# Optimization experiments

Measured on AMD Instinct MI355X. Metric: run time of the kernel, lower is better.

The kernel has to match this reference:

```python
import jax, jax.numpy as jnp
import numpy as np

NUM_HEADS = 32
NUM_GROUP_HEADS = 8
DIM_MODEL = 2048
DIM_K = 64
DIM_V = 64


def setup_inputs() -> dict:
    key = jax.random.key(0)
    ks = jax.random.split(key, 11)
    B, S = 1, 2048
    scale = 0.02
    inp = {
        "queries": jax.random.normal(ks[0], (B, S, DIM_MODEL), jnp.float32),
        "keys": jax.random.normal(ks[1], (B, S, DIM_MODEL), jnp.float32),
        "values": jax.random.normal(ks[2], (B, S, DIM_MODEL), jnp.float32),
        "Wq": jax.random.normal(ks[3], (DIM_MODEL, DIM_K * NUM_HEADS), jnp.float32) * scale,
        "bq": jnp.zeros((DIM_K * NUM_HEADS,), jnp.float32),
        "Wk": jax.random.normal(ks[4], (DIM_MODEL, DIM_K * NUM_GROUP_HEADS), jnp.float32) * scale,
        "bk": jnp.zeros((DIM_K * NUM_GROUP_HEADS,), jnp.float32),
        "Wv": jax.random.normal(ks[5], (DIM_MODEL, DIM_V * NUM_GROUP_HEADS), jnp.float32) * scale,
        "bv": jnp.zeros((DIM_V * NUM_GROUP_HEADS,), jnp.float32),
        "Wo": jax.random.normal(ks[6], (DIM_V * NUM_HEADS, DIM_MODEL), jnp.float32) * scale,
        "bo": jnp.zeros((DIM_MODEL,), jnp.float32),
    }
    return inp


def reference(queries, keys, values, Wq, bq, Wk, bk, Wv, bv, Wo, bo):
    B, Sq, _ = queries.shape
    _, Sk, _ = keys.shape
    H, G = NUM_HEADS, NUM_GROUP_HEADS
    repeats = H // G

    # projections -> [B, heads, S, d]
    q = (queries @ Wq + bq).reshape(B, Sq, H, DIM_K).transpose(0, 2, 1, 3)
    k = (keys @ Wk + bk).reshape(B, Sk, G, DIM_K).transpose(0, 2, 1, 3)
    v = (values @ Wv + bv).reshape(B, Sk, G, DIM_V).transpose(0, 2, 1, 3)

    # GQA: repeat each group head `repeats` times (repeat_interleave on head dim)
    k = jnp.repeat(k, repeats, axis=1)  # [B, H, Sk, dk]
    v = jnp.repeat(v, repeats, axis=1)  # [B, H, Sk, dv]

    scores = jnp.einsum("bhqd,bhkd->bhqk", q, k) / (DIM_K ** 0.5)
    causal = jnp.triu(jnp.ones((Sq, Sk), dtype=bool), k=1)
    scores = jnp.where(causal, -jnp.inf, scores)
    attn = jax.nn.softmax(scores, axis=-1)
    out = jnp.einsum("bhqk,bhkd->bhqd", attn, v)  # [B, H, Sq, dv]
    out = out.transpose(0, 2, 1, 3).reshape(B, Sq, H * DIM_V)
    return out @ Wo + bo
```

## Files before the change

### kernel.cpp

```cpp
#include <hip/hip_runtime.h>
#include <hip/hip_bf16.h>

#define S_LEN  2048
#define DMODEL 2048
#define NH     32
#define NG     8
#define DK     64
#define DV     64

typedef short bf16x8 __attribute__((ext_vector_type(8)));
typedef float f32x4  __attribute__((ext_vector_type(4)));

__device__ __forceinline__ ushort f32_to_bf16(float f) {
    uint u = __float_as_uint(f);
    return (ushort)((u + 0x7fffu + ((u >> 16) & 1u)) >> 16);
}
__device__ __forceinline__ float bf16_to_f32(ushort h) {
    return __uint_as_float(((uint)h) << 16);
}
__device__ __forceinline__ uint pack_bf16x2(float a, float b) {
    return (uint)f32_to_bf16(a) | ((uint)f32_to_bf16(b) << 16);
}

__global__ void cast3_f32_to_bf16(const float* __restrict__ q,
                                  const float* __restrict__ k,
                                  const float* __restrict__ v,
                                  ushort* __restrict__ xq,
                                  ushort* __restrict__ xk,
                                  ushort* __restrict__ xv, int n8) {
    const float* in  = blockIdx.z == 0 ? q  : (blockIdx.z == 1 ? k  : v);
    ushort*      out = blockIdx.z == 0 ? xq : (blockIdx.z == 1 ? xk : xv);
    int i = blockIdx.x * blockDim.x + threadIdx.x;
    const int stride = gridDim.x * blockDim.x;
    for (; i < n8; i += stride) {
        const float4 a = ((const float4*)in)[2 * i];
        const float4 b = ((const float4*)in)[2 * i + 1];
        uint4 o;
        o.x = (uint)f32_to_bf16(a.x) | ((uint)f32_to_bf16(a.y) << 16);
        o.y = (uint)f32_to_bf16(a.z) | ((uint)f32_to_bf16(a.w) << 16);
        o.z = (uint)f32_to_bf16(b.x) | ((uint)f32_to_bf16(b.y) << 16);
        o.w = (uint)f32_to_bf16(b.z) | ((uint)f32_to_bf16(b.w) << 16);
        ((uint4*)out)[i] = o;
    }
}

__global__ void transpose_cast4(const float* __restrict__ Wq,
                                const float* __restrict__ Wk,
                                const float* __restrict__ Wv,
                                const float* __restrict__ Wo,
                                ushort* __restrict__ Wqt, ushort* __restrict__ Wkt,
                                ushort* __restrict__ Wvt, ushort* __restrict__ Wot) {
    __shared__ float t[32][33];
    int bx = blockIdx.x;
    const float* W; ushort* Wt; int N;
    if (bx < 64)      { W = Wq; Wt = Wqt; N = 2048; }
    else if (bx < 80) { W = Wk; Wt = Wkt; N = 512;  bx -= 64; }
    else if (bx < 96) { W = Wv; Wt = Wvt; N = 512;  bx -= 80; }
    else              { W = Wo; Wt = Wot; N = 2048; bx -= 96; }
    const int n0 = bx * 32, k0 = blockIdx.y * 32;
    const int tx = threadIdx.x, ty = threadIdx.y;
#pragma unroll
    for (int i = 0; i < 4; ++i)
        t[ty + 8 * i][tx] = W[(size_t)(k0 + ty + 8 * i) * N + n0 + tx];
    __syncthreads();
#pragma unroll
    for (int i = 0; i < 4; ++i)
        Wt[(size_t)(n0 + ty + 8 * i) * 2048 + k0 + tx] = f32_to_bf16(t[tx][ty + 8 * i]);
}

template <int MODE>
__device__ __forceinline__ void gemm_body_128x64(
        const ushort* __restrict__ A, const ushort* __restrict__ Bt,
        const float* __restrict__ bias, void* __restrict__ Cv,
        ushort* As, ushort* Bs, ushort* Ts, int N, int K, float scale,
        int bx, int by) {
    const int tid  = threadIdx.x;
    const int lane = tid & 63, wave = tid >> 6;
    const int l15 = lane & 15, quad = lane >> 4;
    const int row0 = by * 128, col0 = bx * 64;

    f32x4 acc[2][4];
#pragma unroll
    for (int i = 0; i < 2; ++i)
#pragma unroll
        for (int j = 0; j < 4; ++j) { f32x4 z = {0.f,0.f,0.f,0.f}; acc[i][j] = z; }

    const int ar = tid >> 1, ak = (tid & 1) * 32;
    const int br = tid >> 2, bk = (tid & 3) * 16;
    const ushort* aptr = A  + (size_t)(row0 + ar) * K + ak;
    const ushort* bptr = Bt + (size_t)(col0 + br) * K + bk;

    bf16x8 xa0 = *(const bf16x8*)(aptr);
    bf16x8 xa1 = *(const bf16x8*)(aptr + 8);
    bf16x8 xa2 = *(const bf16x8*)(aptr + 16);
    bf16x8 xa3 = *(const bf16x8*)(aptr + 24);
    bf16x8 xb0 = *(const bf16x8*)(bptr);
    bf16x8 xb1 = *(const bf16x8*)(bptr + 8);
    bf16x8 ya0 = *(const bf16x8*)(aptr + 64);
    bf16x8 ya1 = *(const bf16x8*)(aptr + 72);
    bf16x8 ya2 = *(const bf16x8*)(aptr + 80);
    bf16x8 ya3 = *(const bf16x8*)(aptr + 88);
    bf16x8 yb0 = *(const bf16x8*)(bptr + 64);
    bf16x8 yb1 = *(const bf16x8*)(bptr + 72);

    for (int k0 = 0; k0 < K; k0 += 128) {
        __syncthreads();
        *(bf16x8*)&As[ar * 72 + ak]      = xa0;
        *(bf16x8*)&As[ar * 72 + ak + 8]  = xa1;
        *(bf16x8*)&As[ar * 72 + ak + 16] = xa2;
        *(bf16x8*)&As[ar * 72 + ak + 24] = xa3;
        *(bf16x8*)&Bs[br * 72 + bk]      = xb0;
        *(bf16x8*)&Bs[br * 72 + bk + 8]  = xb1;
        __syncthreads();
        if (k0 + 128 < K) {
            xa0 = *(const bf16x8*)(aptr + k0 + 128);
            xa1 = *(const bf16x8*)(aptr + k0 + 136);
            xa2 = *(const bf16x8*)(aptr + k0 + 144);
            xa3 = *(const bf16x8*)(aptr + k0 + 152);
            xb0 = *(const bf16x8*)(bptr + k0 + 128);
            xb1 = *(const bf16x8*)(bptr + k0 + 136);
        }
#pragma unroll
        for (int kk = 0; kk < 2; ++kk) {
            bf16x8 af[2], bf[4];
#pragma unroll
            for (int mi = 0; mi < 2; ++mi)
                af[mi] = *(const bf16x8*)&As[(wave * 32 + mi * 16 + l15) * 72 + kk * 32 + quad * 8];
#pragma unroll
            for (int ni = 0; ni < 4; ++ni)
                bf[ni] = *(const bf16x8*)&Bs[(ni * 16 + l15) * 72 + kk * 32 + quad * 8];
#pragma unroll
            for (int mi = 0; mi < 2; ++mi)
#pragma unroll
                for (int ni = 0; ni < 4; ++ni)
                    acc[mi][ni] = __builtin_amdgcn_mfma_f32_16x16x32_bf16(
                        af[mi], bf[ni], acc[mi][ni], 0, 0, 0);
        }

        __syncthreads();
        *(bf16x8*)&As[ar * 72 + ak]      = ya0;
        *(bf16x8*)&As[ar * 72 + ak + 8]  = ya1;
        *(bf16x8*)&As[ar * 72 + ak + 16] = ya2;
        *(bf16x8*)&As[ar * 72 + ak + 24] = ya3;
        *(bf16x8*)&Bs[br * 72 + bk]      = yb0;
        *(bf16x8*)&Bs[br * 72 + bk + 8]  = yb1;
        __syncthreads();
        if (k0 + 192 < K) {
            ya0 = *(const bf16x8*)(aptr + k0 + 192);
            ya1 = *(const bf16x8*)(aptr + k0 + 200);
            ya2 = *(const bf16x8*)(aptr + k0 + 208);
            ya3 = *(const bf16x8*)(aptr + k0 + 216);
            yb0 = *(const bf16x8*)(bptr + k0 + 192);
            yb1 = *(const bf16x8*)(bptr + k0 + 200);
        }
#pragma unroll
        for (int kk = 0; kk < 2; ++kk) {
            bf16x8 af[2], bf[4];
#pragma unroll
            for (int mi = 0; mi < 2; ++mi)
                af[mi] = *(const bf16x8*)&As[(wave * 32 + mi * 16 + l15) * 72 + kk * 32 + quad * 8];
#pragma unroll
            for (int ni = 0; ni < 4; ++ni)
                bf[ni] = *(const bf16x8*)&Bs[(ni * 16 + l15) * 72 + kk * 32 + quad * 8];
#pragma unroll
            for (int mi = 0; mi < 2; ++mi)
#pragma unroll
                for (int ni = 0; ni < 4; ++ni)
                    acc[mi][ni] = __builtin_amdgcn_mfma_f32_16x16x32_bf16(
                        af[mi], bf[ni], acc[mi][ni], 0, 0, 0);
        }
    }

    if (MODE == 2) {
        __syncthreads();
#pragma unroll
        for (int mi = 0; mi < 2; ++mi)
#pragma unroll
            for (int ni = 0; ni < 4; ++ni) {
                const float bv = bias[col0 + ni * 16 + l15];
                const int lrow = wave * 32 + mi * 16 + quad * 4;
                uint2 uu;
                uu.x = pack_bf16x2((acc[mi][ni][0] + bv) * scale,
                                   (acc[mi][ni][1] + bv) * scale);
                uu.y = pack_bf16x2((acc[mi][ni][2] + bv) * scale,
                                   (acc[mi][ni][3] + bv) * scale);
                *(uint2*)&Ts[(ni * 16 + l15) * 136 + lrow] = uu;
            }
        __syncthreads();
        const int v = tid >> 2, s0 = (tid & 3) * 32;
#pragma unroll
        for (int i = 0; i < 4; ++i) {
            const uint4 d = *(const uint4*)&Ts[v * 136 + s0 + 8 * i];
            *(uint4*)&((ushort*)Cv)[(size_t)(col0 + v) * S_LEN + row0 + s0 + 8 * i] = d;
        }
        return;
    }

#pragma unroll
    for (int mi = 0; mi < 2; ++mi)
#pragma unroll
        for (int ni = 0; ni < 4; ++ni) {
            const int col = col0 + ni * 16 + l15;
            const float bv = bias[col];
#pragma unroll
            for (int reg = 0; reg < 4; ++reg) {
                const int row = row0 + wave * 32 + mi * 16 + quad * 4 + reg;
                const float val = (acc[mi][ni][reg] + bv) * scale;
                if (MODE == 1)
                    ((float*)Cv)[(size_t)row * N + col] = val;
                else
                    ((ushort*)Cv)[(size_t)row * N + col] = f32_to_bf16(val);
            }
        }
}

__device__ __forceinline__ void xcd_decode_32x16(int d, int& bx, int& by) {
    const int xcd = d & 7, i = d >> 3;
    bx = (xcd & 3) * 8 + (i & 7);
    by = (xcd >> 2) * 8 + (i >> 3);
}

__global__ __launch_bounds__(256) void gemm_q(
        const ushort* __restrict__ A, const ushort* __restrict__ Bt,
        const float* __restrict__ bias, ushort* __restrict__ Cv, int K,
        float scale) {
    __shared__ ushort smem[128 * 72 + 64 * 72];
    int bx, by; xcd_decode_32x16(blockIdx.x, bx, by);
    gemm_body_128x64<0>(A, Bt, bias, Cv, smem, smem + 128 * 72, nullptr,
                        2048, K, scale, bx, by);
}

__global__ __launch_bounds__(256) void gemm_o(
        const ushort* __restrict__ A, const ushort* __restrict__ Bt,
        const float* __restrict__ bias, float* __restrict__ Cv, int K) {
    __shared__ ushort smem[128 * 72 + 64 * 72];
    int bx, by; xcd_decode_32x16(blockIdx.x, bx, by);
    gemm_body_128x64<1>(A, Bt, bias, Cv, smem, smem + 128 * 72, nullptr,
                        2048, K, 1.0f, bx, by);
}

__global__ __launch_bounds__(256) void gemm_kv(
        const ushort* __restrict__ Xk, const ushort* __restrict__ Xv,
        const ushort* __restrict__ Wkt, const ushort* __restrict__ Wvt,
        const float* __restrict__ bk, const float* __restrict__ bv,
        ushort* __restrict__ Kb, ushort* __restrict__ Vtp, int K) {
    __shared__ ushort smem[128 * 72 + 64 * 72];
    ushort* As = smem;
    ushort* Bs = smem + 128 * 72;
    if (blockIdx.z == 0)
        gemm_body_128x64<0>(Xk, Wkt, bk, Kb, As, Bs, nullptr, 512, K, 1.0f,
                            blockIdx.x, blockIdx.y);
    else
        gemm_body_128x64<2>(Xv, Wvt, bv, Vtp, As, Bs, smem, 512, K, 1.0f,
                            blockIdx.x, blockIdx.y);
}

__global__ __launch_bounds__(256) void gqa_attn_mfma(
        const ushort* __restrict__ Qb, const ushort* __restrict__ Kb,
        const ushort* __restrict__ Vt, ushort* __restrict__ Ab) {
    __shared__ ushort Ks[64 * 72];
    __shared__ ushort Vs[64 * 72];
    __shared__ ushort Ps[4][16 * 72];

    const int h    = blockIdx.x, g = h >> 2;
    const int tid  = threadIdx.x;
    const int lane = tid & 63, wave = tid >> 6;
    const int l15  = lane & 15, quad = lane >> 4;
    const int NT   = S_LEN / 64;
    const float DEFER_THR = 11.5416f;

    const int srow = tid >> 2, sch = tid & 3;
    const ushort* kbase = Kb + (size_t)srow * (NG * DK) + g * DK + sch * 16;
    const ushort* vbase = Vt + (size_t)(g * 64 + srow) * S_LEN + sch * 16;

    const int qt = blockIdx.z ? (NT - 1 - (int)blockIdx.y) : (int)blockIdx.y;
    const int qr = qt * 64 + wave * 16;

    bf16x8 qa0, qa1;
    {
        const size_t base = (size_t)(qr + l15) * (NH * DK) + (size_t)h * DK + quad * 8;
        qa0 = *(const bf16x8*)&Qb[base];
        qa1 = *(const bf16x8*)&Qb[base + 32];
    }

    f32x4 o[4];
#pragma unroll
    for (int dt = 0; dt < 4; ++dt) { f32x4 z = {0.f,0.f,0.f,0.f}; o[dt] = z; }
    float m = -1e30f;
    float l = 0.f;

    bf16x8 kr0 = *(const bf16x8*)(kbase);
    bf16x8 kr1 = *(const bf16x8*)(kbase + 8);
    bf16x8 vr0 = *(const bf16x8*)(vbase);
    bf16x8 vr1 = *(const bf16x8*)(vbase + 8);

    for (int jt = 0; jt <= qt; ++jt) {
        __syncthreads();
        *(bf16x8*)&Ks[srow * 72 + sch * 16]     = kr0;
        *(bf16x8*)&Ks[srow * 72 + sch * 16 + 8] = kr1;
        *(bf16x8*)&Vs[srow * 72 + sch * 16]     = vr0;
        *(bf16x8*)&Vs[srow * 72 + sch * 16 + 8] = vr1;
        __syncthreads();

        if (jt < qt) {
            const size_t ko = (size_t)(jt + 1) * 64 * (NG * DK);
            const size_t vo = (size_t)(jt + 1) * 64;
            kr0 = *(const bf16x8*)(kbase + ko);
            kr1 = *(const bf16x8*)(kbase + ko + 8);
            vr0 = *(const bf16x8*)(vbase + vo);
            vr1 = *(const bf16x8*)(vbase + vo + 8);
        }

        f32x4 s[4];
#pragma unroll
        for (int kt = 0; kt < 4; ++kt) {
            const bf16x8 kb0 = *(const bf16x8*)&Ks[(kt * 16 + l15) * 72 + quad * 8];
            const bf16x8 kb1 = *(const bf16x8*)&Ks[(kt * 16 + l15) * 72 + 32 + quad * 8];
            f32x4 acc = {0.f, 0.f, 0.f, 0.f};
            acc = __builtin_amdgcn_mfma_f32_16x16x32_bf16(kb0, qa0, acc, 0, 0, 0);
            acc = __builtin_amdgcn_mfma_f32_16x16x32_bf16(kb1, qa1, acc, 0, 0, 0);
            s[kt] = acc;
        }

        if (jt == qt) {
            const int row = wave * 16 + l15;
#pragma unroll
            for (int kt = 0; kt < 4; ++kt)
#pragma unroll
                for (int r = 0; r < 4; ++r) {
                    const int key = kt * 16 + quad * 4 + r;
                    if (key > row) s[kt][r] = -1e30f;
                }
        }

        float pmax;
        {
            const float t0 = fmaxf(fmaxf(s[0][0], s[0][1]), fmaxf(s[0][2], s[0][3]));
            const float t1 = fmaxf(fmaxf(s[1][0], s[1][1]), fmaxf(s[1][2], s[1][3]));
            const float t2 = fmaxf(fmaxf(s[2][0], s[2][1]), fmaxf(s[2][2], s[2][3]));
            const float t3 = fmaxf(fmaxf(s[3][0], s[3][1]), fmaxf(s[3][2], s[3][3]));
            pmax = fmaxf(fmaxf(t0, t1), fmaxf(t2, t3));
        }
        pmax = fmaxf(pmax, __shfl_xor(pmax, 16, 64));
        pmax = fmaxf(pmax, __shfl_xor(pmax, 32, 64));

        if (!__all(pmax - m <= DEFER_THR)) {
            const float mnew  = fmaxf(m, pmax);
            const float alpha = __builtin_amdgcn_exp2f(m - mnew);
            l *= alpha;
#pragma unroll
            for (int dt = 0; dt < 4; ++dt)
#pragma unroll
                for (int r = 0; r < 4; ++r) o[dt][r] *= alpha;
            m = mnew;
        }

        float p[4][4];
#pragma unroll
        for (int kt = 0; kt < 4; ++kt)
#pragma unroll
            for (int r = 0; r < 4; ++r)
                p[kt][r] = __builtin_amdgcn_exp2f(s[kt][r] - m);

        float rsum;
        {
            const float u0 = (p[0][0] + p[0][1]) + (p[0][2] + p[0][3]);
            const float u1 = (p[1][0] + p[1][1]) + (p[1][2] + p[1][3]);
            const float u2 = (p[2][0] + p[2][1]) + (p[2][2] + p[2][3]);
            const float u3 = (p[3][0] + p[3][1]) + (p[3][2] + p[3][3]);
            rsum = (u0 + u1) + (u2 + u3);
        }
        rsum += __shfl_xor(rsum, 16, 64);
        rsum += __shfl_xor(rsum, 32, 64);
        l += rsum;

        ushort* Pw = &Ps[wave][0];
#pragma unroll
        for (int kt = 0; kt < 4; ++kt) {
            uint2 uu;
            uu.x = pack_bf16x2(p[kt][0], p[kt][1]);
            uu.y = pack_bf16x2(p[kt][2], p[kt][3]);
            *(uint2*)&Pw[l15 * 72 + kt * 16 + quad * 4] = uu;
        }
        const bf16x8 pa0 = *(const bf16x8*)&Pw[l15 * 72 + quad * 8];
        const bf16x8 pa1 = *(const bf16x8*)&Pw[l15 * 72 + 32 + quad * 8];

#pragma unroll
        for (int dt = 0; dt < 4; ++dt) {
            const bf16x8 vb0 = *(const bf16x8*)&Vs[(dt * 16 + l15) * 72 + quad * 8];
            const bf16x8 vb1 = *(const bf16x8*)&Vs[(dt * 16 + l15) * 72 + 32 + quad * 8];
            o[dt] = __builtin_amdgcn_mfma_f32_16x16x32_bf16(vb0, pa0, o[dt], 0, 0, 0);
            o[dt] = __builtin_amdgcn_mfma_f32_16x16x32_bf16(vb1, pa1, o[dt], 0, 0, 0);
        }
    }

    const float invl = 1.0f / l;
#pragma unroll
    for (int dt = 0; dt < 4; ++dt) {
        uint2 uu;
        uu.x = pack_bf16x2(o[dt][0] * invl, o[dt][1] * invl);
        uu.y = pack_bf16x2(o[dt][2] * invl, o[dt][3] * invl);
        *(uint2*)&Ab[(size_t)(qr + l15) * (NH * DV) + (size_t)h * DV + dt * 16 + quad * 4] = uu;
    }
}

extern "C" void kernel_launch(void* const* d_in, const int* in_sizes, int n_in,
                              void* d_out, int out_size, void* d_ws, size_t ws_size,
                              hipStream_t stream) {
    const float* queries = (const float*)d_in[0];
    const float* keys    = (const float*)d_in[1];
    const float* values  = (const float*)d_in[2];
    const float* Wq      = (const float*)d_in[3];
    const float* bq      = (const float*)d_in[4];
    const float* Wk      = (const float*)d_in[5];
    const float* bk      = (const float*)d_in[6];
    const float* Wv      = (const float*)d_in[7];
    const float* bv      = (const float*)d_in[8];
    const float* Wo      = (const float*)d_in[9];
    const float* bo      = (const float*)d_in[10];
    float* out = (float*)d_out;

    const size_t MB = 1024 * 1024;
    unsigned char* w = (unsigned char*)d_ws;
    ushort* Xq  = (ushort*)(w + 0 * MB);
    ushort* Xk  = (ushort*)(w + 8 * MB);
    ushort* Xv  = (ushort*)(w + 16 * MB);
    ushort* Wqt = (ushort*)(w + 24 * MB);
    ushort* Wkt = (ushort*)(w + 32 * MB);
    ushort* Wvt = (ushort*)(w + 34 * MB);
    ushort* Wot = (ushort*)(w + 36 * MB);
    ushort* Qb  = (ushort*)(w + 44 * MB);
    ushort* Kb  = (ushort*)(w + 52 * MB);
    ushort* Vtp = (ushort*)(w + 54 * MB);
    ushort* Ab  = (ushort*)(w + 56 * MB);

    const int n8 = (S_LEN * DMODEL) / 8;
    cast3_f32_to_bf16<<<dim3(1024, 1, 3), 256, 0, stream>>>(
        queries, keys, values, Xq, Xk, Xv, n8);

    dim3 tb(32, 8);
    transpose_cast4<<<dim3(160, 64), tb, 0, stream>>>(
        Wq, Wk, Wv, Wo, Wqt, Wkt, Wvt, Wot);

    const float QSCALE = 0.125f * 1.44269504f;
    gemm_q<<<512, 256, 0, stream>>>(Xq, Wqt, bq, Qb, DMODEL, QSCALE);

    gemm_kv<<<dim3(8, 16, 2), 256, 0, stream>>>(
        Xk, Xv, Wkt, Wvt, bk, bv, Kb, Vtp, DMODEL);

    gqa_attn_mfma<<<dim3(32, 16, 2), 256, 0, stream>>>(Qb, Kb, Vtp, Ab);

    gemm_o<<<512, 256, 0, stream>>>(Ab, Wot, bo, out, DMODEL);
}
```

Baseline: 269.5 us.

## Split attention KV loop across two wave groups and pair causal query tiles per block

The attention kernel now uses 512 threads. Two groups of four waves each process alternating KV tiles for the same 64-row query tile, and their partial softmax states (m, l, o) are merged through shared memory at the end. Each block also handles a short and a long causal query tile one after the other, which replaces the grid z-dimension and balances work across blocks. This halves the grid and adds a merge step plus extra synchronisation, in exchange for more parallelism per query tile and shorter serial KV loops.

```diff
diff --git a/kernel.cpp b/kernel.cpp
--- a/kernel.cpp
+++ b/kernel.cpp
@@ -255,152 +255,186 @@
                             blockIdx.x, blockIdx.y);
 }
 
-__global__ __launch_bounds__(256) void gqa_attn_mfma(
+__global__ __launch_bounds__(512) void gqa_attn_mfma(
         const ushort* __restrict__ Qb, const ushort* __restrict__ Kb,
         const ushort* __restrict__ Vt, ushort* __restrict__ Ab) {
-    __shared__ ushort Ks[64 * 72];
-    __shared__ ushort Vs[64 * 72];
-    __shared__ ushort Ps[4][16 * 72];
+    __shared__ ushort sm[27648];
 
     const int h    = blockIdx.x, g = h >> 2;
+    const int y    = blockIdx.y;
     const int tid  = threadIdx.x;
     const int lane = tid & 63, wave = tid >> 6;
+    const int pg   = wave >> 2;
     const int l15  = lane & 15, quad = lane >> 4;
-    const int NT   = S_LEN / 64;
     const float DEFER_THR = 11.5416f;
 
-    const int srow = tid >> 2, sch = tid & 3;
+    ushort* Ksg = sm + pg * 4608;
+    ushort* Vsg = sm + 9216 + pg * 4608;
+    ushort* Pw  = sm + 18432 + wave * 1152;
+    float*  scr = (float*)sm;
+
+    const int gtid = tid & 255;
+    const int srow = gtid >> 2, sch = gtid & 3;
     const ushort* kbase = Kb + (size_t)srow * (NG * DK) + g * DK + sch * 16;
     const ushort* vbase = Vt + (size_t)(g * 64 + srow) * S_LEN + sch * 16;
-
-    const int qt = blockIdx.z ? (NT - 1 - (int)blockIdx.y) : (int)blockIdx.y;
-    const int qr = qt * 64 + wave * 16;
-
-    bf16x8 qa0, qa1;
-    {
-        const size_t base = (size_t)(qr + l15) * (NH * DK) + (size_t)h * DK + quad * 8;
-        qa0 = *(const bf16x8*)&Qb[base];
-        qa1 = *(const bf16x8*)&Qb[base + 32];
-    }
-
-    f32x4 o[4];
-#pragma unroll
-    for (int dt = 0; dt < 4; ++dt) { f32x4 z = {0.f,0.f,0.f,0.f}; o[dt] = z; }
-    float m = -1e30f;
-    float l = 0.f;
-
-    bf16x8 kr0 = *(const bf16x8*)(kbase);
-    bf16x8 kr1 = *(const bf16x8*)(kbase + 8);
-    bf16x8 vr0 = *(const bf16x8*)(vbase);
-    bf16x8 vr1 = *(const bf16x8*)(vbase + 8);
-
-    for (int jt = 0; jt <= qt; ++jt) {
-        __syncthreads();
-        *(bf16x8*)&Ks[srow * 72 + sch * 16]     = kr0;
-        *(bf16x8*)&Ks[srow * 72 + sch * 16 + 8] = kr1;
-        *(bf16x8*)&Vs[srow * 72 + sch * 16]     = vr0;
-        *(bf16x8*)&Vs[srow * 72 + sch * 16 + 8] = vr1;
-        __syncthreads();
-
-        if (jt < qt) {
-            const size_t ko = (size_t)(jt + 1) * 64 * (NG * DK);
-            const size_t vo = (size_t)(jt + 1) * 64;
-            kr0 = *(const bf16x8*)(kbase + ko);
-            kr1 = *(const bf16x8*)(kbase + ko + 8);
-            vr0 = *(const bf16x8*)(vbase + vo);
-            vr1 = *(const bf16x8*)(vbase + vo + 8);
-        }
-
-        f32x4 s[4];
-#pragma unroll
-        for (int kt = 0; kt < 4; ++kt) {
-            const bf16x8 kb0 = *(const bf16x8*)&Ks[(kt * 16 + l15) * 72 + quad * 8];
-            const bf16x8 kb1 = *(const bf16x8*)&Ks[(kt * 16 + l15) * 72 + 32 + quad * 8];
-            f32x4 acc = {0.f, 0.f, 0.f, 0.f};
-            acc = __builtin_amdgcn_mfma_f32_16x16x32_bf16(kb0, qa0, acc, 0, 0, 0);
-            acc = __builtin_amdgcn_mfma_f32_16x16x32_bf16(kb1, qa1, acc, 0, 0, 0);
-            s[kt] = acc;
-        }
-
-        if (jt == qt) {
-            const int row = wave * 16 + l15;
-#pragma unroll
-            for (int kt = 0; kt < 4; ++kt)
-#pragma unroll
-                for (int r = 0; r < 4; ++r) {
-                    const int key = kt * 16 + quad * 4 + r;
-                    if (key > row) s[kt][r] = -1e30f;
-                }
-        }
-
-        float pmax;
+    const size_t kstep = (size_t)64 * (NG * DK);
+
+    for (int sel = 0; sel < 2; ++sel) {
+        const int qt = sel ? (31 - y) : y;
+        const int qr = qt * 64 + (wave & 3) * 16;
+
+        bf16x8 qa0, qa1;
         {
-            const float t0 = fmaxf(fmaxf(s[0][0], s[0][1]), fmaxf(s[0][2], s[0][3]));
-            const float t1 = fmaxf(fmaxf(s[1][0], s[1][1]), fmaxf(s[1][2], s[1][3]));
-            const float t2 = fmaxf(fmaxf(s[2][0], s[2][1]), fmaxf(s[2][2], s[2][3]));
-            const float t3 = fmaxf(fmaxf(s[3][0], s[3][1]), fmaxf(s[3][2], s[3][3]));
-            pmax = fmaxf(fmaxf(t0, t1), fmaxf(t2, t3));
-        }
-        pmax = fmaxf(pmax, __shfl_xor(pmax, 16, 64));
-        pmax = fmaxf(pmax, __shfl_xor(pmax, 32, 64));
-
-        if (!__all(pmax - m <= DEFER_THR)) {
-            const float mnew  = fmaxf(m, pmax);
-            const float alpha = __builtin_amdgcn_exp2f(m - mnew);
-            l *= alpha;
+            const size_t base = (size_t)(qr + l15) * (NH * DK) + (size_t)h * DK + quad * 8;
+            qa0 = *(const bf16x8*)&Qb[base];
+            qa1 = *(const bf16x8*)&Qb[base + 32];
+        }
+
+        f32x4 o[4];
+#pragma unroll
+        for (int dt = 0; dt < 4; ++dt) { f32x4 z = {0.f,0.f,0.f,0.f}; o[dt] = z; }
+        float m = -1e30f;
+        float l = 0.f;
+
+        bf16x8 kr0 = *(const bf16x8*)(kbase + pg * kstep);
+        bf16x8 kr1 = *(const bf16x8*)(kbase + pg * kstep + 8);
+        bf16x8 vr0 = *(const bf16x8*)(vbase + pg * 64);
+        bf16x8 vr1 = *(const bf16x8*)(vbase + pg * 64 + 8);
+
+        const int iters = (qt >> 1) + 1;
+        for (int it = 0; it < iters; ++it) {
+            const int j = 2 * it + pg;
+
+            __syncthreads();
+            *(bf16x8*)&Ksg[srow * 72 + sch * 16]     = kr0;
+            *(bf16x8*)&Ksg[srow * 72 + sch * 16 + 8] = kr1;
+            *(bf16x8*)&Vsg[srow * 72 + sch * 16]     = vr0;
+            *(bf16x8*)&Vsg[srow * 72 + sch * 16 + 8] = vr1;
+            __syncthreads();
+
+            if (j + 2 <= qt) {
+                const size_t ko = (size_t)(j + 2) * kstep;
+                const size_t vo = (size_t)(j + 2) * 64;
+                kr0 = *(const bf16x8*)(kbase + ko);
+                kr1 = *(const bf16x8*)(kbase + ko + 8);
+                vr0 = *(const bf16x8*)(vbase + vo);
+                vr1 = *(const bf16x8*)(vbase + vo + 8);
+            }
+
+            if (j <= qt) {
+                f32x4 s[4];
+#pragma unroll
+                for (int kt = 0; kt < 4; ++kt) {
+                    const bf16x8 kb0 = *(const bf16x8*)&Ksg[(kt * 16 + l15) * 72 + quad * 8];
+                    const bf16x8 kb1 = *(const bf16x8*)&Ksg[(kt * 16 + l15) * 72 + 32 + quad * 8];
+                    f32x4 acc = {0.f, 0.f, 0.f, 0.f};
+                    acc = __builtin_amdgcn_mfma_f32_16x16x32_bf16(kb0, qa0, acc, 0, 0, 0);
+                    acc = __builtin_amdgcn_mfma_f32_16x16x32_bf16(kb1, qa1, acc, 0, 0, 0);
+                    s[kt] = acc;
+                }
+
+                if (j == qt) {
+                    const int row = (wave & 3) * 16 + l15;
+#pragma unroll
+                    for (int kt = 0; kt < 4; ++kt)
+#pragma unroll
+                        for (int r = 0; r < 4; ++r) {
+                            const int key = kt * 16 + quad * 4 + r;
+                            if (key > row) s[kt][r] = -1e30f;
+                        }
+                }
+
+                float pmax;
+                {
+                    const float t0 = fmaxf(fmaxf(s[0][0], s[0][1]), fmaxf(s[0][2], s[0][3]));
+                    const float t1 = fmaxf(fmaxf(s[1][0], s[1][1]), fmaxf(s[1][2], s[1][3]));
+                    const float t2 = fmaxf(fmaxf(s[2][0], s[2][1]), fmaxf(s[2][2], s[2][3]));
+                    const float t3 = fmaxf(fmaxf(s[3][0], s[3][1]), fmaxf(s[3][2], s[3][3]));
+                    pmax = fmaxf(fmaxf(t0, t1), fmaxf(t2, t3));
+                }
+                pmax = fmaxf(pmax, __shfl_xor(pmax, 16, 64));
+                pmax = fmaxf(pmax, __shfl_xor(pmax, 32, 64));
+
+                if (!__all(pmax - m <= DEFER_THR)) {
+                    const float mnew  = fmaxf(m, pmax);
+                    const float alpha = __builtin_amdgcn_exp2f(m - mnew);
+                    l *= alpha;
+#pragma unroll
+                    for (int dt = 0; dt < 4; ++dt)
+#pragma unroll
+                        for (int r = 0; r < 4; ++r) o[dt][r] *= alpha;
+                    m = mnew;
+                }
+
+                float p[4][4];
+#pragma unroll
+                for (int kt = 0; kt < 4; ++kt)
+#pragma unroll
+                    for (int r = 0; r < 4; ++r)
+                        p[kt][r] = __builtin_amdgcn_exp2f(s[kt][r] - m);
+
+                float rsum;
+                {
+                    const float u0 = (p[0][0] + p[0][1]) + (p[0][2] + p[0][3]);
+                    const float u1 = (p[1][0] + p[1][1]) + (p[1][2] + p[1][3]);
+                    const float u2 = (p[2][0] + p[2][1]) + (p[2][2] + p[2][3]);
+                    const float u3 = (p[3][0] + p[3][1]) + (p[3][2] + p[3][3]);
+                    rsum = (u0 + u1) + (u2 + u3);
+                }
+                rsum += __shfl_xor(rsum, 16, 64);
+                rsum += __shfl_xor(rsum, 32, 64);
+                l += rsum;
+
+#pragma unroll
+                for (int kt = 0; kt < 4; ++kt) {
+                    uint2 uu;
+                    uu.x = pack_bf16x2(p[kt][0], p[kt][1]);
+                    uu.y = pack_bf16x2(p[kt][2], p[kt][3]);
+                    *(uint2*)&Pw[l15 * 72 + kt * 16 + quad * 4] = uu;
+                }
+                const bf16x8 pa0 = *(const bf16x8*)&Pw[l15 * 72 + quad * 8];
+                const bf16x8 pa1 = *(const bf16x8*)&Pw[l15 * 72 + 32 + quad * 8];
+
+#pragma unroll
+                for (int dt = 0; dt < 4; ++dt) {
+                    const bf16x8 vb0 = *(const bf16x8*)&Vsg[(dt * 16 + l15) * 72 + quad * 8];
+                    const bf16x8 vb1 = *(const bf16x8*)&Vsg[(dt * 16 + l15) * 72 + 32 + quad * 8];
+                    o[dt] = __builtin_amdgcn_mfma_f32_16x16x32_bf16(vb0, pa0, o[dt], 0, 0, 0);
+                    o[dt] = __builtin_amdgcn_mfma_f32_16x16x32_bf16(vb1, pa1, o[dt], 0, 0, 0);
+                }
+            }
+        }
+
+        __syncthreads();
+        if (wave >= 4) {
+            float* p = scr + (((wave - 4) * 64 + lane) * 18);
 #pragma unroll
             for (int dt = 0; dt < 4; ++dt)
 #pragma unroll
-                for (int r = 0; r < 4; ++r) o[dt][r] *= alpha;
-            m = mnew;
-        }
-
-        float p[4][4];
-#pragma unroll
-        for (int kt = 0; kt < 4; ++kt)
-#pragma unroll
-            for (int r = 0; r < 4; ++r)
-                p[kt][r] = __builtin_amdgcn_exp2f(s[kt][r] - m);
-
-        float rsum;
-        {
-            const float u0 = (p[0][0] + p[0][1]) + (p[0][2] + p[0][3]);
-            const float u1 = (p[1][0] + p[1][1]) + (p[1][2] + p[1][3]);
-            const float u2 = (p[2][0] + p[2][1]) + (p[2][2] + p[2][3]);
-            const float u3 = (p[3][0] + p[3][1]) + (p[3][2] + p[3][3]);
-            rsum = (u0 + u1) + (u2 + u3);
-        }
-        rsum += __shfl_xor(rsum, 16, 64);
-        rsum += __shfl_xor(rsum, 32, 64);
-        l += rsum;
-
-        ushort* Pw = &Ps[wave][0];
-#pragma unroll
-        for (int kt = 0; kt < 4; ++kt) {
-            uint2 uu;
-            uu.x = pack_bf16x2(p[kt][0], p[kt][1]);
-            uu.y = pack_bf16x2(p[kt][2], p[kt][3]);
-            *(uint2*)&Pw[l15 * 72 + kt * 16 + quad * 4] = uu;
-        }
-        const bf16x8 pa0 = *(const bf16x8*)&Pw[l15 * 72 + quad * 8];
-        const bf16x8 pa1 = *(const bf16x8*)&Pw[l15 * 72 + 32 + quad * 8];
-
-#pragma unroll
-        for (int dt = 0; dt < 4; ++dt) {
-            const bf16x8 vb0 = *(const bf16x8*)&Vs[(dt * 16 + l15) * 72 + quad * 8];
-            const bf16x8 vb1 = *(const bf16x8*)&Vs[(dt * 16 + l15) * 72 + 32 + quad * 8];
-            o[dt] = __builtin_amdgcn_mfma_f32_16x16x32_bf16(vb0, pa0, o[dt], 0, 0, 0);
-            o[dt] = __builtin_amdgcn_mfma_f32_16x16x32_bf16(vb1, pa1, o[dt], 0, 0, 0);
-        }
-    }
-
-    const float invl = 1.0f / l;
-#pragma unroll
-    for (int dt = 0; dt < 4; ++dt) {
-        uint2 uu;
-        uu.x = pack_bf16x2(o[dt][0] * invl, o[dt][1] * invl);
-        uu.y = pack_bf16x2(o[dt][2] * invl, o[dt][3] * invl);
-        *(uint2*)&Ab[(size_t)(qr + l15) * (NH * DV) + (size_t)h * DV + dt * 16 + quad * 4] = uu;
+                for (int r = 0; r < 4; ++r) p[dt * 4 + r] = o[dt][r];
+            p[16] = m;
+            p[17] = l;
+        }
+        __syncthreads();
+        if (wave < 4) {
+            const float* p = scr + ((wave * 64 + lane) * 18);
+            const float m1 = p[16], l1 = p[17];
+            const float M  = fmaxf(m, m1);
+            const float a0 = __builtin_amdgcn_exp2f(m - M);
+            const float a1 = __builtin_amdgcn_exp2f(m1 - M);
+            const float invL = 1.0f / (l * a0 + l1 * a1);
+#pragma unroll
+            for (int dt = 0; dt < 4; ++dt) {
+                float v0 = (o[dt][0] * a0 + p[dt * 4 + 0] * a1) * invL;
+                float v1 = (o[dt][1] * a0 + p[dt * 4 + 1] * a1) * invL;
+                float v2 = (o[dt][2] * a0 + p[dt * 4 + 2] * a1) * invL;
+                float v3 = (o[dt][3] * a0 + p[dt * 4 + 3] * a1) * invL;
+                uint2 uu;
+                uu.x = pack_bf16x2(v0, v1);
+                uu.y = pack_bf16x2(v2, v3);
+                *(uint2*)&Ab[(size_t)(qr + l15) * (NH * DV) + (size_t)h * DV + dt * 16 + quad * 4] = uu;
+            }
+        }
     }
 }
 
@@ -448,7 +482,7 @@
     gemm_kv<<<dim3(8, 16, 2), 256, 0, stream>>>(
         Xk, Xv, Wkt, Wvt, bk, bv, Kb, Vtp, DMODEL);
 
-    gqa_attn_mfma<<<dim3(32, 16, 2), 256, 0, stream>>>(Qb, Kb, Vtp, Ab);
+    gqa_attn_mfma<<<dim3(32, 16), 512, 0, stream>>>(Qb, Kb, Vtp, Ab);
 
     gemm_o<<<512, 256, 0, stream>>>(Ab, Wot, bo, out, DMODEL);
 }
```

After: 268.0 us. No clear change (-0.6%).

## Widen attention key tile to 128 and pair causal query tiles per block

Applied to the files above, without the earlier changes.

The attention kernel now processes 128 keys per iteration instead of 64, which halves the number of barrier/load rounds and softmax reductions per query tile. Each block also handles two query tiles (y and 31-y) in sequence, balancing causal work and halving the grid to 512 blocks. The cost is more shared memory and registers per block, less parallelism from the smaller grid, and masking work wasted on the diagonal 128-key tile for even query tiles.

```diff
diff --git a/kernel.cpp b/kernel.cpp
--- a/kernel.cpp
+++ b/kernel.cpp
@@ -258,149 +258,151 @@
 __global__ __launch_bounds__(256) void gqa_attn_mfma(
         const ushort* __restrict__ Qb, const ushort* __restrict__ Kb,
         const ushort* __restrict__ Vt, ushort* __restrict__ Ab) {
-    __shared__ ushort Ks[64 * 72];
-    __shared__ ushort Vs[64 * 72];
-    __shared__ ushort Ps[4][16 * 72];
+    __shared__ ushort Ks[128 * 72];
+    __shared__ ushort Vs[64 * 136];
+    __shared__ ushort Ps[4][16 * 136];
 
     const int h    = blockIdx.x, g = h >> 2;
+    const int y    = blockIdx.y;
     const int tid  = threadIdx.x;
     const int lane = tid & 63, wave = tid >> 6;
     const int l15  = lane & 15, quad = lane >> 4;
-    const int NT   = S_LEN / 64;
     const float DEFER_THR = 11.5416f;
 
-    const int srow = tid >> 2, sch = tid & 3;
-    const ushort* kbase = Kb + (size_t)srow * (NG * DK) + g * DK + sch * 16;
-    const ushort* vbase = Vt + (size_t)(g * 64 + srow) * S_LEN + sch * 16;
-
-    const int qt = blockIdx.z ? (NT - 1 - (int)blockIdx.y) : (int)blockIdx.y;
-    const int qr = qt * 64 + wave * 16;
-
-    bf16x8 qa0, qa1;
-    {
-        const size_t base = (size_t)(qr + l15) * (NH * DK) + (size_t)h * DK + quad * 8;
-        qa0 = *(const bf16x8*)&Qb[base];
-        qa1 = *(const bf16x8*)&Qb[base + 32];
-    }
-
-    f32x4 o[4];
-#pragma unroll
-    for (int dt = 0; dt < 4; ++dt) { f32x4 z = {0.f,0.f,0.f,0.f}; o[dt] = z; }
-    float m = -1e30f;
-    float l = 0.f;
-
-    bf16x8 kr0 = *(const bf16x8*)(kbase);
-    bf16x8 kr1 = *(const bf16x8*)(kbase + 8);
-    bf16x8 vr0 = *(const bf16x8*)(vbase);
-    bf16x8 vr1 = *(const bf16x8*)(vbase + 8);
-
-    for (int jt = 0; jt <= qt; ++jt) {
-        __syncthreads();
-        *(bf16x8*)&Ks[srow * 72 + sch * 16]     = kr0;
-        *(bf16x8*)&Ks[srow * 72 + sch * 16 + 8] = kr1;
-        *(bf16x8*)&Vs[srow * 72 + sch * 16]     = vr0;
-        *(bf16x8*)&Vs[srow * 72 + sch * 16 + 8] = vr1;
-        __syncthreads();
-
-        if (jt < qt) {
-            const size_t ko = (size_t)(jt + 1) * 64 * (NG * DK);
-            const size_t vo = (size_t)(jt + 1) * 64;
-            kr0 = *(const bf16x8*)(kbase + ko);
-            kr1 = *(const bf16x8*)(kbase + ko + 8);
-            vr0 = *(const bf16x8*)(vbase + vo);
-            vr1 = *(const bf16x8*)(vbase + vo + 8);
-        }
-
-        f32x4 s[4];
-#pragma unroll
-        for (int kt = 0; kt < 4; ++kt) {
-            const bf16x8 kb0 = *(const bf16x8*)&Ks[(kt * 16 + l15) * 72 + quad * 8];
-            const bf16x8 kb1 = *(const bf16x8*)&Ks[(kt * 16 + l15) * 72 + 32 + quad * 8];
-            f32x4 acc = {0.f, 0.f, 0.f, 0.f};
-            acc = __builtin_amdgcn_mfma_f32_16x16x32_bf16(kb0, qa0, acc, 0, 0, 0);
-            acc = __builtin_amdgcn_mfma_f32_16x16x32_bf16(kb1, qa1, acc, 0, 0, 0);
-            s[kt] = acc;
-        }
-
-        if (jt == qt) {
-            const int row = wave * 16 + l15;
-#pragma unroll
-            for (int kt = 0; kt < 4; ++kt)
-#pragma unroll
-                for (int r = 0; r < 4; ++r) {
-                    const int key = kt * 16 + quad * 4 + r;
-                    if (key > row) s[kt][r] = -1e30f;
+    const int krow = tid >> 1, kch = (tid & 1) * 32;
+    const int vrow = tid >> 2, vch = (tid & 3) * 32;
+    const ushort* kbase = Kb + (size_t)krow * (NG * DK) + g * DK + kch;
+    const ushort* vbase = Vt + (size_t)(g * 64 + vrow) * S_LEN + vch;
+    const size_t krstep = (size_t)(NG * DK);
+
+    for (int sel = 0; sel < 2; ++sel) {
+        const int qt = sel ? (31 - y) : y;
+        const int qr = qt * 64 + wave * 16;
+        const int roff = (qt & 1) ? 64 : 0;
+        const int iters = (qt >> 1) + 1;
+
+        bf16x8 qa0, qa1;
+        {
+            const size_t base = (size_t)(qr + l15) * (NH * DK) + (size_t)h * DK + quad * 8;
+            qa0 = *(const bf16x8*)&Qb[base];
+            qa1 = *(const bf16x8*)&Qb[base + 32];
+        }
+
+        f32x4 o[4];
+#pragma unroll
+        for (int dt = 0; dt < 4; ++dt) { f32x4 z = {0.f,0.f,0.f,0.f}; o[dt] = z; }
+        float m = -1e30f;
+        float l = 0.f;
+
+        bf16x8 kr[4], vr[4];
+#pragma unroll
+        for (int i = 0; i < 4; ++i) {
+            kr[i] = *(const bf16x8*)(kbase + 8 * i);
+            vr[i] = *(const bf16x8*)(vbase + 8 * i);
+        }
+
+        for (int it = 0; it < iters; ++it) {
+            __syncthreads();
+#pragma unroll
+            for (int i = 0; i < 4; ++i) {
+                *(bf16x8*)&Ks[krow * 72 + kch + 8 * i]  = kr[i];
+                *(bf16x8*)&Vs[vrow * 136 + vch + 8 * i] = vr[i];
+            }
+            __syncthreads();
+
+            if (it + 1 < iters) {
+                const size_t ko = (size_t)(it + 1) * 128 * krstep;
+                const size_t vo = (size_t)(it + 1) * 128;
+#pragma unroll
+                for (int i = 0; i < 4; ++i) {
+                    kr[i] = *(const bf16x8*)(kbase + ko + 8 * i);
+                    vr[i] = *(const bf16x8*)(vbase + vo + 8 * i);
                 }
-        }
-
-        float pmax;
-        {
-            const float t0 = fmaxf(fmaxf(s[0][0], s[0][1]), fmaxf(s[0][2], s[0][3]));
-            const float t1 = fmaxf(fmaxf(s[1][0], s[1][1]), fmaxf(s[1][2], s[1][3]));
-            const float t2 = fmaxf(fmaxf(s[2][0], s[2][1]), fmaxf(s[2][2], s[2][3]));
-            const float t3 = fmaxf(fmaxf(s[3][0], s[3][1]), fmaxf(s[3][2], s[3][3]));
-            pmax = fmaxf(fmaxf(t0, t1), fmaxf(t2, t3));
-        }
-        pmax = fmaxf(pmax, __shfl_xor(pmax, 16, 64));
-        pmax = fmaxf(pmax, __shfl_xor(pmax, 32, 64));
-
-        if (!__all(pmax - m <= DEFER_THR)) {
-            const float mnew  = fmaxf(m, pmax);
-            const float alpha = __builtin_amdgcn_exp2f(m - mnew);
-            l *= alpha;
-#pragma unroll
-            for (int dt = 0; dt < 4; ++dt)
-#pragma unroll
-                for (int r = 0; r < 4; ++r) o[dt][r] *= alpha;
-            m = mnew;
-        }
-
-        float p[4][4];
-#pragma unroll
-        for (int kt = 0; kt < 4; ++kt)
-#pragma unroll
-            for (int r = 0; r < 4; ++r)
-                p[kt][r] = __builtin_amdgcn_exp2f(s[kt][r] - m);
-
-        float rsum;
-        {
-            const float u0 = (p[0][0] + p[0][1]) + (p[0][2] + p[0][3]);
-            const float u1 = (p[1][0] + p[1][1]) + (p[1][2] + p[1][3]);
-            const float u2 = (p[2][0] + p[2][1]) + (p[2][2] + p[2][3]);
-            const float u3 = (p[3][0] + p[3][1]) + (p[3][2] + p[3][3]);
-            rsum = (u0 + u1) + (u2 + u3);
-        }
-        rsum += __shfl_xor(rsum, 16, 64);
-        rsum += __shfl_xor(rsum, 32, 64);
-        l += rsum;
-
-        ushort* Pw = &Ps[wave][0];
-#pragma unroll
-        for (int kt = 0; kt < 4; ++kt) {
+            }
+
+            f32x4 s[8];
+#pragma unroll
+            for (int kt = 0; kt < 8; ++kt) {
+                const bf16x8 kb0 = *(const bf16x8*)&Ks[(kt * 16 + l15) * 72 + quad * 8];
+                const bf16x8 kb1 = *(const bf16x8*)&Ks[(kt * 16 + l15) * 72 + 32 + quad * 8];
+                f32x4 acc = {0.f, 0.f, 0.f, 0.f};
+                acc = __builtin_amdgcn_mfma_f32_16x16x32_bf16(kb0, qa0, acc, 0, 0, 0);
+                acc = __builtin_amdgcn_mfma_f32_16x16x32_bf16(kb1, qa1, acc, 0, 0, 0);
+                s[kt] = acc;
+            }
+
+            if (it == iters - 1) {
+                const int row = wave * 16 + l15 + roff;
+#pragma unroll
+                for (int kt = 0; kt < 8; ++kt)
+#pragma unroll
+                    for (int r = 0; r < 4; ++r) {
+                        const int key = kt * 16 + quad * 4 + r;
+                        if (key > row) s[kt][r] = -1e30f;
+                    }
+            }
+
+            float pmax;
+            {
+                float t[8];
+#pragma unroll
+                for (int kt = 0; kt < 8; ++kt)
+                    t[kt] = fmaxf(fmaxf(s[kt][0], s[kt][1]), fmaxf(s[kt][2], s[kt][3]));
+                const float u0 = fmaxf(fmaxf(t[0], t[1]), fmaxf(t[2], t[3]));
+                const float u1 = fmaxf(fmaxf(t[4], t[5]), fmaxf(t[6], t[7]));
+                pmax = fmaxf(u0, u1);
+            }
+            pmax = fmaxf(pmax, __shfl_xor(pmax, 16, 64));
+            pmax = fmaxf(pmax, __shfl_xor(pmax, 32, 64));
+
+            if (!__all(pmax - m <= DEFER_THR)) {
+                const float mnew  = fmaxf(m, pmax);
+                const float alpha = __builtin_amdgcn_exp2f(m - mnew);
+                l *= alpha;
+#pragma unroll
+                for (int dt = 0; dt < 4; ++dt)
+#pragma unroll
+                    for (int r = 0; r < 4; ++r) o[dt][r] *= alpha;
+                m = mnew;
+            }
+
+            ushort* Pw = &Ps[wave][0];
+            float rsum = 0.f;
+#pragma unroll
+            for (int kt = 0; kt < 8; ++kt) {
+                const float p0 = __builtin_amdgcn_exp2f(s[kt][0] - m);
+                const float p1 = __builtin_amdgcn_exp2f(s[kt][1] - m);
+                const float p2 = __builtin_amdgcn_exp2f(s[kt][2] - m);
+                const float p3 = __builtin_amdgcn_exp2f(s[kt][3] - m);
+                rsum += (p0 + p1) + (p2 + p3);
+                uint2 uu;
+                uu.x = pack_bf16x2(p0, p1);
+                uu.y = pack_bf16x2(p2, p3);
+                *(uint2*)&Pw[l15 * 136 + kt * 16 + quad * 4] = uu;
+            }
+            rsum += __shfl_xor(rsum, 16, 64);
+            rsum += __shfl_xor(rsum, 32, 64);
+            l += rsum;
+
+#pragma unroll
+            for (int kc = 0; kc < 4; ++kc) {
+                const bf16x8 pa = *(const bf16x8*)&Pw[l15 * 136 + kc * 32 + quad * 8];
+#pragma unroll
+                for (int dt = 0; dt < 4; ++dt) {
+                    const bf16x8 vb = *(const bf16x8*)&Vs[(dt * 16 + l15) * 136 + kc * 32 + quad * 8];
+                    o[dt] = __builtin_amdgcn_mfma_f32_16x16x32_bf16(vb, pa, o[dt], 0, 0, 0);
+                }
+            }
+        }
+
+        const float invl = 1.0f / l;
+#pragma unroll
+        for (int dt = 0; dt < 4; ++dt) {
             uint2 uu;
-            uu.x = pack_bf16x2(p[kt][0], p[kt][1]);
-            uu.y = pack_bf16x2(p[kt][2], p[kt][3]);
-            *(uint2*)&Pw[l15 * 72 + kt * 16 + quad * 4] = uu;
-        }
-        const bf16x8 pa0 = *(const bf16x8*)&Pw[l15 * 72 + quad * 8];
-        const bf16x8 pa1 = *(const bf16x8*)&Pw[l15 * 72 + 32 + quad * 8];
-
-#pragma unroll
-        for (int dt = 0; dt < 4; ++dt) {
-            const bf16x8 vb0 = *(const bf16x8*)&Vs[(dt * 16 + l15) * 72 + quad * 8];
-            const bf16x8 vb1 = *(const bf16x8*)&Vs[(dt * 16 + l15) * 72 + 32 + quad * 8];
-            o[dt] = __builtin_amdgcn_mfma_f32_16x16x32_bf16(vb0, pa0, o[dt], 0, 0, 0);
-            o[dt] = __builtin_amdgcn_mfma_f32_16x16x32_bf16(vb1, pa1, o[dt], 0, 0, 0);
-        }
-    }
-
-    const float invl = 1.0f / l;
-#pragma unroll
-    for (int dt = 0; dt < 4; ++dt) {
-        uint2 uu;
-        uu.x = pack_bf16x2(o[dt][0] * invl, o[dt][1] * invl);
-        uu.y = pack_bf16x2(o[dt][2] * invl, o[dt][3] * invl);
-        *(uint2*)&Ab[(size_t)(qr + l15) * (NH * DV) + (size_t)h * DV + dt * 16 + quad * 4] = uu;
+            uu.x = pack_bf16x2(o[dt][0] * invl, o[dt][1] * invl);
+            uu.y = pack_bf16x2(o[dt][2] * invl, o[dt][3] * invl);
+            *(uint2*)&Ab[(size_t)(qr + l15) * (NH * DV) + (size_t)h * DV + dt * 16 + quad * 4] = uu;
+        }
     }
 }
 
@@ -448,7 +450,7 @@
     gemm_kv<<<dim3(8, 16, 2), 256, 0, stream>>>(
         Xk, Xv, Wkt, Wvt, bk, bv, Kb, Vtp, DMODEL);
 
-    gqa_attn_mfma<<<dim3(32, 16, 2), 256, 0, stream>>>(Qb, Kb, Vtp, Ab);
+    gqa_attn_mfma<<<dim3(32, 16), 256, 0, stream>>>(Qb, Kb, Vtp, Ab);
 
     gemm_o<<<512, 256, 0, stream>>>(Ab, Wot, bo, out, DMODEL);
 }
```

After: 274.9 us. Within noise of the previous version (+2.0%).
